# Performance work log

Hardware: AMD Instinct MI355X
Metric: run time of the kernel (lower is better)

Reference implementation:

```python
import jax, jax.numpy as jnp
import numpy as np

TAU = 2.0
SUR_ALPHA = 4.0  # spikingjelly surrogate.Sigmoid default alpha
LN_EPS = 1e-5
SCALE = 0.125
NUM_HEADS = 16


@jax.custom_vjp
def _spike(u):
    return (u >= 0.0).astype(u.dtype)

def _spike_fwd(u):
    return _spike(u), u

def _spike_bwd(u, g):
    s = jax.nn.sigmoid(SUR_ALPHA * u)
    return (g * SUR_ALPHA * s * (1.0 - s),)

_spike.defvjp(_spike_fwd, _spike_bwd)


def lif(x, v_th=1.0):
    # Single-step LIF from fresh state v=0, v_reset=0:
    # v_post = v + (x - v)/tau = x/tau; spike = H(v_post - v_th)
    return _spike(x / TAU - v_th)


def ln(x, g, b):
    m = jnp.mean(x, axis=-1, keepdims=True)
    v = jnp.var(x, axis=-1, keepdims=True)
    return (x - m) * jax.lax.rsqrt(v + LN_EPS) * g + b


def setup_inputs() -> dict:
    key = jax.random.key(0)
    ks = jax.random.split(key, 8)
    B, L, D = 4, 1024, 1024
    HID = 4096
    s_d = 1.0 / np.sqrt(D)
    s_h = 1.0 / np.sqrt(HID)
    return {
        "x": jax.random.normal(ks[0], (B, L, D), jnp.float32),
        "q_w": jax.random.normal(ks[1], (D, D), jnp.float32) * s_d,
        "q_g": jnp.ones((D,), jnp.float32),
        "q_b": jnp.zeros((D,), jnp.float32),
        "k_w": jax.random.normal(ks[2], (D, D), jnp.float32) * s_d,
        "k_g": jnp.ones((D,), jnp.float32),
        "k_b": jnp.zeros((D,), jnp.float32),
        "v_w": jax.random.normal(ks[3], (D, D), jnp.float32) * s_d,
        "v_g": jnp.ones((D,), jnp.float32),
        "v_b": jnp.zeros((D,), jnp.float32),
        "proj_w": jax.random.normal(ks[4], (D, D), jnp.float32) * s_d,
        "proj_bias": jnp.zeros((D,), jnp.float32),
        "proj_g": jnp.ones((D,), jnp.float32),
        "proj_beta": jnp.zeros((D,), jnp.float32),
        "fc1_w": jax.random.normal(ks[5], (D, HID), jnp.float32) * s_d,
        "fc1_bias": jnp.zeros((HID,), jnp.float32),
        "fc1_g": jnp.ones((HID,), jnp.float32),
        "fc1_beta": jnp.zeros((HID,), jnp.float32),
        "fc2_w": jax.random.normal(ks[6], (HID, D), jnp.float32) * s_h,
        "fc2_bias": jnp.zeros((D,), jnp.float32),
        "fc2_g": jnp.ones((D,), jnp.float32),
        "fc2_beta": jnp.zeros((D,), jnp.float32),
    }


def reference(x, q_w, q_g, q_b, k_w, k_g, k_b, v_w, v_g, v_b,
              proj_w, proj_bias, proj_g, proj_beta,
              fc1_w, fc1_bias, fc1_g, fc1_beta,
              fc2_w, fc2_bias, fc2_g, fc2_beta):
    B, L, D = x.shape
    H = NUM_HEADS
    hd = D // H

    # --- SSA ---
    q = lif(ln(x @ q_w, q_g, q_b))  # (B,L,D), binary spikes
    k = lif(ln(x @ k_w, k_g, k_b))
    v = lif(ln(x @ v_w, v_g, v_b))
    q = q.reshape(B, L, H, hd).transpose(0, 2, 1, 3)  # (B,H,L,hd)
    k = k.reshape(B, L, H, hd).transpose(0, 2, 1, 3)
    v = v.reshape(B, L, H, hd).transpose(0, 2, 1, 3)

    attn = jnp.einsum('bhqd,bhkd->bhqk', q, k) * SCALE  # no softmax
    y = jnp.einsum('bhqk,bhkd->bhqd', attn, v)
    y = y.transpose(0, 2, 1, 3).reshape(B, L, D)
    y = lif(y, v_th=0.5)                    # attn_lif (v_threshold=0.5)
    y = lif(ln(y @ proj_w + proj_bias, proj_g, proj_beta))

    x = x + y  # residual 1

    # --- MLP ---
    m = lif(ln(x @ fc1_w + fc1_bias, fc1_g, fc1_beta))
    m = lif(ln(m @ fc2_w + fc2_bias, fc2_g, fc2_beta))

    return x + m  # residual 2
```

## Files before the change

### kernel.cpp

```cpp
#include <hip/hip_runtime.h>
#include <hip/hip_bf16.h>


#define NB 4
#define LL 1024
#define DIM 1024
#define NH 16
#define HDIM 64
#define HID 4096
#define NROWS (NB * LL)

typedef unsigned short u16;
typedef __attribute__((ext_vector_type(8))) short short8v;
typedef __attribute__((ext_vector_type(4))) float f32x4;

__device__ __forceinline__ u16 f2bf(float f) {
    unsigned u = __builtin_bit_cast(unsigned, f);
    return (u16)((u + 0x7fffu + ((u >> 16) & 1u)) >> 16);
}
__device__ __forceinline__ float bf2f(u16 h) {
    unsigned u = ((unsigned)h) << 16;
    return __builtin_bit_cast(float, u);
}
__device__ __forceinline__ void split3v(float v, u16& a, u16& b, u16& c) {
    a = f2bf(v);
    float r = v - bf2f(a);
    b = f2bf(r);
    float r2 = r - bf2f(b);
    c = f2bf(r2);
}

__global__ __launch_bounds__(256) void split3_rows(
    const float* __restrict__ X, u16* __restrict__ Xs, int K)
{
    const int row = blockIdx.y;
    const int c4 = (blockIdx.x * 256 + threadIdx.x) * 4;
    if (c4 >= K) return;
    float4 v = *(const float4*)(X + (size_t)row * K + c4);
    float vv[4] = {v.x, v.y, v.z, v.w};
    u16 h0[4], h1[4], h2[4];
#pragma unroll
    for (int j = 0; j < 4; ++j) split3v(vv[j], h0[j], h1[j], h2[j]);
    u16* base = Xs + (size_t)row * 3 * K + c4;
    *(uint2*)(base + 0 * K) = *(uint2*)h0;
    *(uint2*)(base + 1 * K) = *(uint2*)h1;
    *(uint2*)(base + 2 * K) = *(uint2*)h2;
}

__global__ __launch_bounds__(256) void split_wt(
    const float* __restrict__ W, u16* __restrict__ Wt, int K, int N, int ldwt)
{
    __shared__ float tile[64][65];
    const int k0 = blockIdx.y * 64, n0 = blockIdx.x * 64;
    const int t = threadIdx.x;
    const int rr = t >> 4;
    const int cc = (t & 15) * 4;
#pragma unroll
    for (int it = 0; it < 4; ++it) {
        const int k = rr + it * 16;
        float4 v = *(const float4*)(W + (size_t)(k0 + k) * N + n0 + cc);
        tile[cc + 0][k] = v.x; tile[cc + 1][k] = v.y;
        tile[cc + 2][k] = v.z; tile[cc + 3][k] = v.w;
    }
    __syncthreads();
    const int n = t >> 2, kc = (t & 3) * 16;
    u16 h0[16], h1[16], h2[16];
#pragma unroll
    for (int j = 0; j < 16; ++j)
        split3v(tile[n][kc + j], h0[j], h1[j], h2[j]);
    u16* base = Wt + (size_t)(n0 + n) * ldwt + k0 + kc;
    *(uint4*)(base + 0 * K)     = ((uint4*)h0)[0];
    *(uint4*)(base + 0 * K + 8) = ((uint4*)h0)[1];
    *(uint4*)(base + 1 * K)     = ((uint4*)h1)[0];
    *(uint4*)(base + 1 * K + 8) = ((uint4*)h1)[1];
    *(uint4*)(base + 2 * K)     = ((uint4*)h2)[0];
    *(uint4*)(base + 2 * K + 8) = ((uint4*)h2)[1];
}

#define AS1G const __attribute__((address_space(1))) void*
#define AS3L __attribute__((address_space(3))) void*

__global__ __launch_bounds__(512, 2) void gemm256(
    const u16* __restrict__ A, int lda,
    const u16* __restrict__ Bt, int ldb,
    unsigned apack, unsigned bpack, int nt,
    const float* __restrict__ bias,
    float* __restrict__ Out, int ldo)
{
    __shared__ u16 As2[2][16384];
    __shared__ u16 Bs2[2][16384];
    const int t = threadIdx.x;
    const int wid = t >> 6, lane = t & 63;
    const int wm = wid >> 2, wn = wid & 3;
    int bid = blockIdx.y * gridDim.x + blockIdx.x;
    const int nwg = gridDim.x * gridDim.y;
    bid = (bid & 7) * (nwg >> 3) + (bid >> 3);
    const int row0 = (bid / gridDim.x) * 256, col0 = (bid % gridDim.x) * 256;
    const int lrow = lane & 15, lk = lane >> 4;
    const int sr0 = t >> 3;
    const int scol = ((t & 7) ^ (sr0 & 7)) * 8;

    f32x4 acc[8][4];
#pragma unroll
    for (int i = 0; i < 8; ++i)
#pragma unroll
        for (int j = 0; j < 4; ++j) acc[i][j] = f32x4{0.f, 0.f, 0.f, 0.f};
    short8v afA[4][2], afB[4][2], bf[2][2];

#define STA(bs, Rb, c0)                                                        \
    __builtin_amdgcn_global_load_lds(                                          \
        (AS1G)(A + (size_t)(row0 + (Rb) + sr0) * lda + (c0) + scol),           \
        (AS3L)(&As2[bs][(Rb) * 64 + t * 8]), 16, 0, 0);
#define STB(bs, Rb, c0)                                                        \
    {                                                                          \
        const int _rho = (Rb) + sr0;                                           \
        const int _bc = ((_rho >> 5) & 3) * 64 + ((_rho >> 7) << 5) + (_rho & 31); \
        __builtin_amdgcn_global_load_lds(                                      \
            (AS1G)(Bt + (size_t)(col0 + _bc) * ldb + (c0) + scol),             \
            (AS3L)(&Bs2[bs][(Rb) * 64 + t * 8]), 16, 0, 0);                    \
    }
#define STPAIR0(bs, cA, cB) STA(bs, 0, cA)   STA(bs, 128, cA)
#define STPAIR1(bs, cA, cB) STB(bs, 0, cB)   STB(bs, 64, cB)
#define STPAIR2(bs, cA, cB) STA(bs, 64, cA)  STA(bs, 192, cA)
#define STPAIR3(bs, cA, cB) STB(bs, 128, cB) STB(bs, 192, cB)

#define VMW(n) asm volatile("s_waitcnt vmcnt(" #n ")" ::: "memory");
#define BAR  __builtin_amdgcn_s_barrier();
#define BARP                                                                   \
    __builtin_amdgcn_s_barrier();                                              \
    __builtin_amdgcn_sched_barrier(0);
#define LGKM0                                                                  \
    asm volatile("s_waitcnt lgkmcnt(0)" ::: "memory");                         \
    __builtin_amdgcn_sched_barrier(0);

#define LDA(dst, MQ, P)                                                        \
    _Pragma("unroll")                                                          \
    for (int mf = 0; mf < 4; ++mf) {                                           \
        const int r = wm * 128 + (MQ) * 64 + mf * 16 + lrow;                   \
        _Pragma("unroll")                                                      \
        for (int ks = 0; ks < 2; ++ks) {                                       \
            const int slot = (lk + ks * 4) ^ (r & 7);                          \
            dst[mf][ks] = *(const short8v*)&As2[P][r * 64 + slot * 8];         \
        }                                                                      \
    }
#define LDB(NQ, P)                                                             \
    _Pragma("unroll")                                                          \
    for (int nf = 0; nf < 2; ++nf) {                                           \
        const int rho = (NQ) * 128 + (wn >> 1) * 64 + (wn & 1) * 32            \
                        + nf * 16 + lrow;                                      \
        _Pragma("unroll")                                                      \
        for (int ks = 0; ks < 2; ++ks) {                                       \
            const int slot = (lk + ks * 4) ^ (rho & 7);                        \
            bf[nf][ks] = *(const short8v*)&Bs2[P][rho * 64 + slot * 8];        \
        }                                                                      \
    }
#define MM(asrc, MQ, NQ)                                                       \
    __builtin_amdgcn_s_setprio(1);                                             \
    _Pragma("unroll")                                                          \
    for (int mf = 0; mf < 4; ++mf)                                             \
        _Pragma("unroll")                                                      \
        for (int nf = 0; nf < 2; ++nf)                                         \
            _Pragma("unroll")                                                  \
            for (int ks = 0; ks < 2; ++ks)                                     \
                acc[(MQ) * 4 + mf][(NQ) * 2 + nf] =                            \
                    __builtin_amdgcn_mfma_f32_16x16x32_bf16(                   \
                        asrc[mf][ks], bf[nf][ks],                              \
                        acc[(MQ) * 4 + mf][(NQ) * 2 + nf], 0, 0, 0);           \
    __builtin_amdgcn_s_setprio(0);

    {
        const int cA = (apack & 15) * 1024;
        const int cB = (bpack & 15) * 1024;
        STPAIR0(0, cA, cB) STPAIR1(0, cA, cB)
        STPAIR2(0, cA, cB) STPAIR3(0, cA, cB)
    }

    for (int kt = 0; kt < nt - 1; ++kt) {
        const int p = kt & 1, np = p ^ 1;
        const int nkt = kt + 1;
        const int nns = nkt >> 4, nk0 = (nkt & 15) * 64;
        const int nA = (int)((apack >> (nns * 4)) & 15) * 1024 + nk0;
        const int nB = (int)((bpack >> (nns * 4)) & 15) * 1024 + nk0;
        VMW(4) BARP
        LDA(afA, 0, p) LDB(0, p) STPAIR0(np, nA, nB) LGKM0 MM(afA, 0, 0)
        VMW(4) BAR
        LDA(afB, 1, p) STPAIR1(np, nA, nB) LGKM0 MM(afB, 1, 0)
        VMW(4) BAR
        LDB(1, p) STPAIR2(np, nA, nB) LGKM0 MM(afB, 1, 1)
        BAR
        STPAIR3(np, nA, nB) MM(afA, 0, 1)
    }
    {
        const int p = (nt - 1) & 1;
        VMW(4) BARP LDA(afA, 0, p) LDB(0, p) LGKM0 MM(afA, 0, 0)
        VMW(2) BAR  LDA(afB, 1, p) LGKM0 MM(afB, 1, 0)
        VMW(0) BAR  LDB(1, p) LGKM0 MM(afB, 1, 1)
        BAR         MM(afA, 0, 1)
    }
#undef STA
#undef STB
#undef STPAIR0
#undef STPAIR1
#undef STPAIR2
#undef STPAIR3
#undef VMW
#undef BAR
#undef BARP
#undef LGKM0
#undef LDA
#undef LDB
#undef MM

#pragma unroll
    for (int ni = 0; ni < 4; ++ni) {
        const int col = col0 + wn * 64 + ni * 16 + lrow;
        const float bv = bias ? bias[col] : 0.f;
#pragma unroll
        for (int mi = 0; mi < 8; ++mi) {
            const int rbase = row0 + wm * 128 + mi * 16 + lk * 4;
#pragma unroll
            for (int r = 0; r < 4; ++r)
                Out[(size_t)(rbase + r) * ldo + col] = acc[mi][ni][r] + bv;
        }
    }
}

struct SegList { int a[6]; int b[6]; int n; };

template <int BN_>
__global__ __launch_bounds__(256) void gemm_mfma(
    const u16* __restrict__ A, int lda,
    const u16* __restrict__ Bt, int ldb,
    SegList segs, int Kseg,
    const float* __restrict__ bias,
    float* __restrict__ Out, int ldo)
{
    constexpr int NF = BN_ / 32;
    __shared__ u16 As[128 * 64];
    __shared__ u16 Bs[BN_ * 64];
    const int t = threadIdx.x;
    const int wid = t >> 6, lane = t & 63;
    const int wr = wid >> 1, wc = wid & 1;
    int bid = blockIdx.y * gridDim.x + blockIdx.x;
    const int nwg = gridDim.x * gridDim.y;
    bid = (bid & 7) * (nwg >> 3) + (bid >> 3);
    const int row0 = (bid / gridDim.x) * 128, col0 = (bid % gridDim.x) * BN_;
    const int lrow = lane & 15;
    const int s_subrow = lane >> 3;
    const int s_slot   = (lane & 7) ^ (lane >> 3);
    const int s_coff   = s_slot * 8;

    f32x4 acc[4][NF];
#pragma unroll
    for (int i = 0; i < 4; ++i)
#pragma unroll
        for (int j = 0; j < NF; ++j) acc[i][j] = f32x4{0.f, 0.f, 0.f, 0.f};

    for (int s = 0; s < segs.n; ++s) {
        const u16* pa = A + segs.a[s];
        const u16* pb = Bt + segs.b[s];
        for (int k0 = 0; k0 < Kseg; k0 += 64) {
            asm volatile("s_waitcnt lgkmcnt(0)" ::: "memory");
            __syncthreads();
#pragma unroll
            for (int c = 0; c < 4; ++c) {
                const int chunk = wid * 4 + c;
                const int rg = row0 + chunk * 8 + s_subrow;
                __builtin_amdgcn_global_load_lds(
                    (AS1G)(pa + (size_t)rg * lda + k0 + s_coff),
                    (AS3L)(&As[chunk * 512 + lane * 8]), 16, 0, 0);
            }
#pragma unroll
            for (int c = 0; c < NF; ++c) {
                const int chunk = wid * NF + c;
                const int rg = col0 + chunk * 8 + s_subrow;
                __builtin_amdgcn_global_load_lds(
                    (AS1G)(pb + (size_t)rg * ldb + k0 + s_coff),
                    (AS3L)(&Bs[chunk * 512 + lane * 8]), 16, 0, 0);
            }
            asm volatile("s_waitcnt vmcnt(0)" ::: "memory");
            __syncthreads();
#pragma unroll
            for (int ksub = 0; ksub < 2; ++ksub) {
                short8v af[4], bfr[NF];
#pragma unroll
                for (int f = 0; f < 4; ++f) {
                    const int ra = wr * 64 + f * 16 + lrow;
                    const int slot = ((lane >> 4) + ksub * 4) ^ (lrow & 7);
                    af[f] = *(const short8v*)&As[ra * 64 + slot * 8];
                }
#pragma unroll
                for (int f = 0; f < NF; ++f) {
                    const int rb = wc * (BN_ / 2) + f * 16 + lrow;
                    const int slot = ((lane >> 4) + ksub * 4) ^ (lrow & 7);
                    bfr[f] = *(const short8v*)&Bs[rb * 64 + slot * 8];
                }
#pragma unroll
                for (int i = 0; i < 4; ++i)
#pragma unroll
                    for (int j = 0; j < NF; ++j)
                        acc[i][j] = __builtin_amdgcn_mfma_f32_16x16x32_bf16(
                            af[i], bfr[j], acc[i][j], 0, 0, 0);
            }
        }
    }
#pragma unroll
    for (int j = 0; j < NF; ++j) {
        const int col = col0 + wc * (BN_ / 2) + j * 16 + lrow;
        const float bv = bias ? bias[col] : 0.f;
#pragma unroll
        for (int i = 0; i < 4; ++i) {
            const int rbase = row0 + wr * 64 + i * 16 + (lane >> 4) * 4;
#pragma unroll
            for (int r = 0; r < 4; ++r)
                Out[(size_t)(rbase + r) * ldo + col] = acc[i][j][r] + bv;
        }
    }
}

template <int DN>
__global__ __launch_bounds__(256) void lnlif2(
    const float* __restrict__ U, int ld, int coloff,
    const float* __restrict__ g, const float* __restrict__ beta,
    const float* __restrict__ resid,
    u16* __restrict__ spike_bf16,
    float* __restrict__ out_f32,
    u16* __restrict__ split3_out)
{
    constexpr int PT = DN / 1024;
    const int r = blockIdx.x, t = threadIdx.x;
    const float4* u4 = (const float4*)(U + (size_t)r * ld + coloff);
    float4 vals[PT];
    float lsum = 0.f;
#pragma unroll
    for (int i = 0; i < PT; ++i) {
        vals[i] = u4[t + i * 256];
        lsum += (vals[i].x + vals[i].y) + (vals[i].z + vals[i].w);
    }
    __shared__ float red[4];
    __shared__ float bcast;
    for (int o = 32; o > 0; o >>= 1) lsum += __shfl_down(lsum, o);
    if ((t & 63) == 0) red[t >> 6] = lsum;
    __syncthreads();
    if (t == 0) bcast = (red[0] + red[1] + red[2] + red[3]) * (1.f / DN);
    __syncthreads();
    const float m = bcast;
    float lss = 0.f;
#pragma unroll
    for (int i = 0; i < PT; ++i) {
        float dx = vals[i].x - m, dy = vals[i].y - m;
        float dz = vals[i].z - m, dw = vals[i].w - m;
        lss += (dx * dx + dy * dy) + (dz * dz + dw * dw);
    }
    for (int o = 32; o > 0; o >>= 1) lss += __shfl_down(lss, o);
    if ((t & 63) == 0) red[t >> 6] = lss;
    __syncthreads();
    if (t == 0) bcast = (red[0] + red[1] + red[2] + red[3]) * (1.f / DN);
    __syncthreads();
    const float rs = 1.f / sqrtf(bcast + 1e-5f);
#pragma unroll
    for (int i = 0; i < PT; ++i) {
        const int c = (t + i * 256) * 4;
        const size_t idx = (size_t)r * DN + c;
        const float4 gg = *(const float4*)(g + c);
        const float4 bb = *(const float4*)(beta + c);
        float sv[4];
        sv[0] = ((vals[i].x - m) * rs * gg.x + bb.x >= 2.0f) ? 1.f : 0.f;
        sv[1] = ((vals[i].y - m) * rs * gg.y + bb.y >= 2.0f) ? 1.f : 0.f;
        sv[2] = ((vals[i].z - m) * rs * gg.z + bb.z >= 2.0f) ? 1.f : 0.f;
        sv[3] = ((vals[i].w - m) * rs * gg.w + bb.w >= 2.0f) ? 1.f : 0.f;
        if (spike_bf16) {
            u16 sp[4];
#pragma unroll
            for (int j = 0; j < 4; ++j) sp[j] = sv[j] != 0.f ? (u16)0x3F80 : (u16)0;
            *(uint2*)(spike_bf16 + idx) = *(uint2*)sp;
        }
        if (out_f32 || split3_out) {
            float4 rv = resid ? *(const float4*)(resid + idx)
                              : float4{0.f, 0.f, 0.f, 0.f};
            float vv[4] = {rv.x + sv[0], rv.y + sv[1], rv.z + sv[2], rv.w + sv[3]};
            if (out_f32) {
                float4 ov = {vv[0], vv[1], vv[2], vv[3]};
                *(float4*)(out_f32 + idx) = ov;
            }
            if (split3_out) {
                u16 h0[4], h1[4], h2[4];
#pragma unroll
                for (int j = 0; j < 4; ++j) split3v(vv[j], h0[j], h1[j], h2[j]);
                u16* base = split3_out + (size_t)r * 3 * DN + c;
                *(uint2*)(base + 0 * DN) = *(uint2*)h0;
                *(uint2*)(base + 1 * DN) = *(uint2*)h1;
                *(uint2*)(base + 2 * DN) = *(uint2*)h2;
            }
        }
    }
}

__global__ __launch_bounds__(256) void ktv_part(
    const u16* __restrict__ Sk, const u16* __restrict__ Sv,
    float* __restrict__ ktvp)
{
    const int bh = blockIdx.x, ck = blockIdx.y;
    const int b = bh >> 4, h = bh & 15;
    __shared__ float kch[64][64];
    __shared__ float vch[64][64];
    const int t = threadIdx.x;
    const int i = t >> 2;
    const int j0 = (t & 3) << 4;
    float4 a0 = {0,0,0,0}, a1 = {0,0,0,0}, a2 = {0,0,0,0}, a3 = {0,0,0,0};
    for (int l0 = ck * 256; l0 < ck * 256 + 256; l0 += 64) {
        __syncthreads();
#pragma unroll
        for (int q = 0; q < 2; ++q) {
            const int chunk = t + q * 256;
            const int li = chunk >> 3, c8 = (chunk & 7) << 3;
            const size_t off = ((size_t)b * LL + l0 + li) * DIM + h * HDIM + c8;
            union { uint4 v; u16 s[8]; } uk, uv;
            uk.v = *(const uint4*)(Sk + off);
            uv.v = *(const uint4*)(Sv + off);
#pragma unroll
            for (int j = 0; j < 8; ++j) {
                kch[li][c8 + j] = uk.s[j] ? 1.f : 0.f;
                vch[li][c8 + j] = uv.s[j] ? 1.f : 0.f;
            }
        }
        __syncthreads();
        for (int l = 0; l < 64; ++l) {
            if (kch[l][i] != 0.f) {
                const float4 v0 = *(float4*)&vch[l][j0];
                const float4 v1 = *(float4*)&vch[l][j0 + 4];
                const float4 v2 = *(float4*)&vch[l][j0 + 8];
                const float4 v3 = *(float4*)&vch[l][j0 + 12];
                a0.x += v0.x; a0.y += v0.y; a0.z += v0.z; a0.w += v0.w;
                a1.x += v1.x; a1.y += v1.y; a1.z += v1.z; a1.w += v1.w;
                a2.x += v2.x; a2.y += v2.y; a2.z += v2.z; a2.w += v2.w;
                a3.x += v3.x; a3.y += v3.y; a3.z += v3.z; a3.w += v3.w;
            }
        }
    }
    const size_t o = (((size_t)ck * 64 + bh) * 64 + i) * 64 + j0;
    *(float4*)(ktvp + o)      = a0;
    *(float4*)(ktvp + o + 4)  = a1;
    *(float4*)(ktvp + o + 8)  = a2;
    *(float4*)(ktvp + o + 12) = a3;
}

__global__ __launch_bounds__(256) void qktv_bf16(
    const u16* __restrict__ Sq, const float* __restrict__ ktvp,
    u16* __restrict__ Y)
{
    const int bh = blockIdx.x, ck = blockIdx.y;
    const int b = bh >> 4, h = bh & 15;
    __shared__ float kt[64][64];
    const int t = threadIdx.x;
#pragma unroll
    for (int q = 0; q < 16; ++q) {
        const int idx = t + q * 256;
        ((float*)kt)[idx] = (ktvp[((size_t)0 * 64 + bh) * 4096 + idx]
                           + ktvp[((size_t)1 * 64 + bh) * 4096 + idx])
                          + (ktvp[((size_t)2 * 64 + bh) * 4096 + idx]
                           + ktvp[((size_t)3 * 64 + bh) * 4096 + idx]);
    }
    __syncthreads();
    const int li = t >> 6;
    const int j = t & 63;
    for (int l0 = ck * 128; l0 < ck * 128 + 128; l0 += 4) {
        const size_t roff = ((size_t)b * LL + l0 + li) * DIM + h * HDIM;
        const u16 sqv = Sq[roff + j];
        unsigned long long mask = __ballot(sqv != 0);
        float acc = 0.f;
        while (mask) {
            const int i = __ffsll((unsigned long long)mask) - 1;
            mask &= mask - 1;
            acc += kt[i][j];
        }
        const float y = 0.125f * acc;
        Y[roff + j] = (y >= 1.0f) ? (u16)0x3F80 : (u16)0;
    }
}

#define BM 128
#define BN 128
#define BK 16

__global__ __launch_bounds__(256) void gemm_f32(
    const float* __restrict__ A, const float* __restrict__ W,
    const float* __restrict__ bias, float* __restrict__ U,
    int M, int K, int N)
{
    __shared__ float As[BK][BM];
    __shared__ float Bs[BK][BN];
    const int t = threadIdx.x;
    const int tx = t & 15, ty = t >> 4;
    const int row0 = blockIdx.y * BM, col0 = blockIdx.x * BN;
    const int ar = t >> 2;
    const int ac = (t & 3) << 2;
    const int br = t >> 5;
    const int bc = (t & 31) << 2;
    float acc[8][8];
#pragma unroll
    for (int i = 0; i < 8; ++i)
#pragma unroll
        for (int j = 0; j < 8; ++j) acc[i][j] = 0.f;
    for (int k0 = 0; k0 < K; k0 += BK) {
        float4 va0 = *(const float4*)(A + (size_t)(row0 + ar) * K + k0 + ac);
        float4 va1 = *(const float4*)(A + (size_t)(row0 + ar + 64) * K + k0 + ac);
        float4 vb0 = *(const float4*)(W + (size_t)(k0 + br) * N + col0 + bc);
        float4 vb1 = *(const float4*)(W + (size_t)(k0 + br + 8) * N + col0 + bc);
        __syncthreads();
        As[ac + 0][ar] = va0.x; As[ac + 1][ar] = va0.y;
        As[ac + 2][ar] = va0.z; As[ac + 3][ar] = va0.w;
        As[ac + 0][ar + 64] = va1.x; As[ac + 1][ar + 64] = va1.y;
        As[ac + 2][ar + 64] = va1.z; As[ac + 3][ar + 64] = va1.w;
        *(float4*)&Bs[br][bc] = vb0;
        *(float4*)&Bs[br + 8][bc] = vb1;
        __syncthreads();
#pragma unroll
        for (int kk = 0; kk < BK; ++kk) {
            float4 fa0 = *(float4*)&As[kk][ty * 8];
            float4 fa1 = *(float4*)&As[kk][ty * 8 + 4];
            float4 fb0 = *(float4*)&Bs[kk][tx * 8];
            float4 fb1 = *(float4*)&Bs[kk][tx * 8 + 4];
            float av[8] = {fa0.x, fa0.y, fa0.z, fa0.w, fa1.x, fa1.y, fa1.z, fa1.w};
            float bv[8] = {fb0.x, fb0.y, fb0.z, fb0.w, fb1.x, fb1.y, fb1.z, fb1.w};
#pragma unroll
            for (int i = 0; i < 8; ++i)
#pragma unroll
                for (int j = 0; j < 8; ++j)
                    acc[i][j] += av[i] * bv[j];
        }
    }
    float bvals[8];
#pragma unroll
    for (int j = 0; j < 8; ++j)
        bvals[j] = bias ? bias[col0 + tx * 8 + j] : 0.f;
#pragma unroll
    for (int i = 0; i < 8; ++i) {
        const int row = row0 + ty * 8 + i;
        float* dst = U + (size_t)row * N + col0 + tx * 8;
        float4 o0, o1;
        o0.x = acc[i][0] + bvals[0]; o0.y = acc[i][1] + bvals[1];
        o0.z = acc[i][2] + bvals[2]; o0.w = acc[i][3] + bvals[3];
        o1.x = acc[i][4] + bvals[4]; o1.y = acc[i][5] + bvals[5];
        o1.z = acc[i][6] + bvals[6]; o1.w = acc[i][7] + bvals[7];
        *(float4*)dst = o0;
        *(float4*)(dst + 4) = o1;
    }
}

template <int DN>
__global__ __launch_bounds__(256) void lnlif_old(
    const float* __restrict__ U, const float* __restrict__ g,
    const float* __restrict__ beta, float thr,
    const float* __restrict__ resid, float* __restrict__ out)
{
    constexpr int PT = DN / 256;
    const int r = blockIdx.x, t = threadIdx.x;
    const float* u = U + (size_t)r * DN;
    float vals[PT];
    float lsum = 0.f;
#pragma unroll
    for (int i = 0; i < PT; ++i) { vals[i] = u[t + i * 256]; lsum += vals[i]; }
    __shared__ float red[4];
    __shared__ float bc0;
    for (int o = 32; o > 0; o >>= 1) lsum += __shfl_down(lsum, o);
    if ((t & 63) == 0) red[t >> 6] = lsum;
    __syncthreads();
    if (t == 0) bc0 = (red[0] + red[1] + red[2] + red[3]) * (1.f / DN);
    __syncthreads();
    const float m = bc0;
    float lss = 0.f;
#pragma unroll
    for (int i = 0; i < PT; ++i) { float d = vals[i] - m; lss += d * d; }
    for (int o = 32; o > 0; o >>= 1) lss += __shfl_down(lss, o);
    if ((t & 63) == 0) red[t >> 6] = lss;
    __syncthreads();
    if (t == 0) bc0 = (red[0] + red[1] + red[2] + red[3]) * (1.f / DN);
    __syncthreads();
    const float rs = 1.0f / sqrtf(bc0 + 1e-5f);
#pragma unroll
    for (int i = 0; i < PT; ++i) {
        const int c = t + i * 256;
        const float nrm = (vals[i] - m) * rs * g[c] + beta[c];
        const float s = (nrm >= thr) ? 1.0f : 0.0f;
        out[(size_t)r * DN + c] = resid ? (resid[(size_t)r * DN + c] + s) : s;
    }
}

__global__ __launch_bounds__(256) void ktv_f32(
    const float* __restrict__ Sk, const float* __restrict__ Sv,
    float* __restrict__ ktvb)
{
    const int bh = blockIdx.x;
    const int b = bh >> 4, h = bh & 15;
    __shared__ float kch[64][64];
    __shared__ float vch[64][64];
    const int t = threadIdx.x;
    const int i = t >> 2;
    const int j0 = (t & 3) << 4;
    float4 a0 = {0,0,0,0}, a1 = {0,0,0,0}, a2 = {0,0,0,0}, a3 = {0,0,0,0};
    for (int l0 = 0; l0 < LL; l0 += 64) {
        __syncthreads();
#pragma unroll
        for (int q = 0; q < 4; ++q) {
            const int idx = t + q * 256;
            const int li = idx >> 4, c4 = (idx & 15) << 2;
            const size_t off = ((size_t)b * LL + l0 + li) * DIM + h * HDIM + c4;
            *(float4*)&kch[li][c4] = *(const float4*)(Sk + off);
            *(float4*)&vch[li][c4] = *(const float4*)(Sv + off);
        }
        __syncthreads();
        for (int l = 0; l < 64; ++l) {
            if (kch[l][i] != 0.f) {
                const float4 v0 = *(float4*)&vch[l][j0];
                const float4 v1 = *(float4*)&vch[l][j0 + 4];
                const float4 v2 = *(float4*)&vch[l][j0 + 8];
                const float4 v3 = *(float4*)&vch[l][j0 + 12];
                a0.x += v0.x; a0.y += v0.y; a0.z += v0.z; a0.w += v0.w;
                a1.x += v1.x; a1.y += v1.y; a1.z += v1.z; a1.w += v1.w;
                a2.x += v2.x; a2.y += v2.y; a2.z += v2.z; a2.w += v2.w;
                a3.x += v3.x; a3.y += v3.y; a3.z += v3.z; a3.w += v3.w;
            }
        }
    }
    const size_t o = ((size_t)bh * 64 + i) * 64 + j0;
    *(float4*)(ktvb + o)      = a0;
    *(float4*)(ktvb + o + 4)  = a1;
    *(float4*)(ktvb + o + 8)  = a2;
    *(float4*)(ktvb + o + 12) = a3;
}

__global__ __launch_bounds__(256) void qktv_f32(
    const float* __restrict__ Sq, const float* __restrict__ ktvb,
    float* __restrict__ Y)
{
    const int bh = blockIdx.x;
    const int b = bh >> 4, h = bh & 15;
    __shared__ float kt[64][64];
    const int t = threadIdx.x;
#pragma unroll
    for (int q = 0; q < 16; ++q) {
        const int idx = t + q * 256;
        ((float*)kt)[idx] = ktvb[(size_t)bh * 4096 + idx];
    }
    __syncthreads();
    const int li = t >> 6;
    const int j = t & 63;
    for (int l0 = 0; l0 < LL; l0 += 4) {
        const size_t roff = ((size_t)b * LL + l0 + li) * DIM + h * HDIM;
        const float sqv = Sq[roff + j];
        unsigned long long mask = __ballot(sqv != 0.f);
        float acc = 0.f;
        while (mask) {
            const int i = __ffsll((unsigned long long)mask) - 1;
            mask &= mask - 1;
            acc += kt[i][j];
        }
        const float y = 0.125f * acc;
        Y[roff + j] = (y >= 1.0f) ? 1.0f : 0.0f;
    }
}

extern "C" void kernel_launch(void* const* d_in, const int* in_sizes, int n_in,
                              void* d_out, int out_size, void* d_ws, size_t ws_size,
                              hipStream_t stream)
{
    const float* x        = (const float*)d_in[0];
    const float* q_w      = (const float*)d_in[1];
    const float* q_g      = (const float*)d_in[2];
    const float* q_b      = (const float*)d_in[3];
    const float* k_w      = (const float*)d_in[4];
    const float* k_g      = (const float*)d_in[5];
    const float* k_b      = (const float*)d_in[6];
    const float* v_w      = (const float*)d_in[7];
    const float* v_g      = (const float*)d_in[8];
    const float* v_b      = (const float*)d_in[9];
    const float* proj_w   = (const float*)d_in[10];
    const float* proj_bias= (const float*)d_in[11];
    const float* proj_g   = (const float*)d_in[12];
    const float* proj_beta= (const float*)d_in[13];
    const float* fc1_w    = (const float*)d_in[14];
    const float* fc1_bias = (const float*)d_in[15];
    const float* fc1_g    = (const float*)d_in[16];
    const float* fc1_beta = (const float*)d_in[17];
    const float* fc2_w    = (const float*)d_in[18];
    const float* fc2_bias = (const float*)d_in[19];
    const float* fc2_g    = (const float*)d_in[20];
    const float* fc2_beta = (const float*)d_in[21];

    const dim3 blk(256);
    const size_t NEEDED = 143654912;

    if (ws_size >= NEEDED) {
        char* ws = (char*)d_ws;
        float* U    = (float*)ws;
        u16*   Xsh  = (u16*)(ws + 67108864);
        u16*   Wbuf = (u16*)(ws + 100663296);
        u16*   Sq   = (u16*)(ws + 125829120);
        u16*   Sk   = (u16*)(ws + 134217728);
        u16*   SvYb = (u16*)((char*)Xsh + 25165824);
        u16*   Xs   = Xsh;
        u16*   X1s  = Xsh;
        u16*   Sm   = Xsh;
        float* X1   = (float*)d_out;
        float* ktvp = (float*)(ws + 100663296);

        const int pa6[6] = {0, 1, 2, 0, 1, 0}, pb6[6] = {0, 1, 0, 2, 0, 1};
        unsigned apack = 0, bpack = 0;
        for (int i = 0; i < 6; ++i) {
            apack |= (unsigned)pa6[i] << (4 * i);
            bpack |= (unsigned)pb6[i] << (4 * i);
        }
        SegList segP;
        {
            for (int i = 0; i < 6; ++i) { segP.a[i] = 0; segP.b[i] = 0; }
            segP.b[1] = 1024; segP.b[2] = 2048; segP.n = 3;
        }
        SegList segF2;
        {
            for (int i = 0; i < 6; ++i) { segF2.a[i] = 0; segF2.b[i] = 0; }
            segF2.b[1] = 4096; segF2.b[2] = 8192; segF2.n = 3;
        }

        split3_rows<<<dim3(1, NROWS), blk, 0, stream>>>(x, Xs, DIM);

        split_wt<<<dim3(16, 16), blk, 0, stream>>>(q_w, Wbuf,               DIM, DIM, 3072);
        split_wt<<<dim3(16, 16), blk, 0, stream>>>(k_w, Wbuf + 1024 * 3072, DIM, DIM, 3072);
        split_wt<<<dim3(16, 16), blk, 0, stream>>>(v_w, Wbuf + 2048 * 3072, DIM, DIM, 3072);
        gemm256<<<dim3(12, 16), dim3(512), 0, stream>>>(
            Xs, 3072, Wbuf, 3072, apack, bpack, 96, nullptr, U, 3072);
        lnlif2<DIM><<<NROWS, blk, 0, stream>>>(U, 3072, 0,    q_g, q_b, nullptr, Sq,   nullptr, nullptr);
        lnlif2<DIM><<<NROWS, blk, 0, stream>>>(U, 3072, 1024, k_g, k_b, nullptr, Sk,   nullptr, nullptr);
        lnlif2<DIM><<<NROWS, blk, 0, stream>>>(U, 3072, 2048, v_g, v_b, nullptr, SvYb, nullptr, nullptr);

        ktv_part<<<dim3(NB * NH, 4), blk, 0, stream>>>(Sk, SvYb, ktvp);
        qktv_bf16<<<dim3(NB * NH, 8), blk, 0, stream>>>(Sq, ktvp, SvYb);

        split_wt<<<dim3(16, 16), blk, 0, stream>>>(proj_w, Wbuf, DIM, DIM, 3072);
        gemm_mfma<128><<<dim3(8, 32), blk, 0, stream>>>(SvYb, 1024, Wbuf, 3072, segP, 1024, proj_bias, U, DIM);
        lnlif2<DIM><<<NROWS, blk, 0, stream>>>(U, DIM, 0, proj_g, proj_beta, x, nullptr, X1, X1s);

        split_wt<<<dim3(64, 16), blk, 0, stream>>>(fc1_w, Wbuf, DIM, HID, 3072);
        gemm256<<<dim3(16, 16), dim3(512), 0, stream>>>(
            X1s, 3072, Wbuf, 3072, apack, bpack, 96, fc1_bias, U, HID);
        lnlif2<HID><<<NROWS, blk, 0, stream>>>(U, HID, 0, fc1_g, fc1_beta, nullptr, Sm, nullptr, nullptr);

        split_wt<<<dim3(16, 64), blk, 0, stream>>>(fc2_w, Wbuf, HID, DIM, 12288);
        gemm_mfma<128><<<dim3(8, 32), blk, 0, stream>>>(Sm, 4096, Wbuf, 12288, segF2, 4096, fc2_bias, U, DIM);
        lnlif2<DIM><<<NROWS, blk, 0, stream>>>(U, DIM, 0, fc2_g, fc2_beta, X1, nullptr, (float*)d_out, nullptr);
        return;
    }

    float* U    = (float*)d_ws;
    float* Sq   = U + (size_t)1 * NROWS * DIM;
    float* Sk   = U + (size_t)2 * NROWS * DIM;
    float* Sv   = U + (size_t)3 * NROWS * DIM;
    float* Yb   = Sv;
    float* ktvb = U + (size_t)NROWS * HID;
    float* Y2   = ktvb + (size_t)NB * NH * HDIM * HDIM;
    float* X1   = (float*)d_out;
    float* outf = (float*)d_out;

    const dim3 gemm_d(DIM / BN, NROWS / BM);
    const dim3 gemm_h(HID / BN, NROWS / BM);

    gemm_f32<<<gemm_d, blk, 0, stream>>>(x, q_w, nullptr, U, NROWS, DIM, DIM);
    lnlif_old<DIM><<<NROWS, blk, 0, stream>>>(U, q_g, q_b, 2.0f, nullptr, Sq);
    gemm_f32<<<gemm_d, blk, 0, stream>>>(x, k_w, nullptr, U, NROWS, DIM, DIM);
    lnlif_old<DIM><<<NROWS, blk, 0, stream>>>(U, k_g, k_b, 2.0f, nullptr, Sk);
    gemm_f32<<<gemm_d, blk, 0, stream>>>(x, v_w, nullptr, U, NROWS, DIM, DIM);
    lnlif_old<DIM><<<NROWS, blk, 0, stream>>>(U, v_g, v_b, 2.0f, nullptr, Sv);

    ktv_f32<<<NB * NH, blk, 0, stream>>>(Sk, Sv, ktvb);
    qktv_f32<<<NB * NH, blk, 0, stream>>>(Sq, ktvb, Yb);

    gemm_f32<<<gemm_d, blk, 0, stream>>>(Yb, proj_w, proj_bias, U, NROWS, DIM, DIM);
    lnlif_old<DIM><<<NROWS, blk, 0, stream>>>(U, proj_g, proj_beta, 2.0f, x, X1);

    gemm_f32<<<gemm_h, blk, 0, stream>>>(X1, fc1_w, fc1_bias, U, NROWS, DIM, HID);
    lnlif_old<HID><<<NROWS, blk, 0, stream>>>(U, fc1_g, fc1_beta, 2.0f, nullptr, U);

    gemm_f32<<<gemm_d, blk, 0, stream>>>(U, fc2_w, fc2_bias, Y2, NROWS, HID, DIM);
    lnlif_old<DIM><<<NROWS, blk, 0, stream>>>(Y2, fc2_g, fc2_beta, 2.0f, X1, outf);
}
```

Baseline: 686.6 us.

## Replace proj/fc2 GEMM with double-buffered 128x128 pipelined MFMA kernel

Swaps the simple single-buffered gemm_mfma used for the proj and fc2 spike GEMMs for a new gemm128p kernel. The new kernel double-buffers LDS and interleaves async global-to-LDS loads for the next K tile with MFMA work on the current one, using split vmcnt waits, s_setprio and sched barriers, as the gemm256 kernel already does. Segment offsets are packed into a bitfield so the three bf16 weight splits are walked as one continuous K loop. It doubles LDS use per block and adds scheduling complexity, which may lower occupancy.

```diff
diff --git a/kernel.cpp b/kernel.cpp
--- a/kernel.cpp
+++ b/kernel.cpp
@@ -197,16 +197,156 @@
         VMW(0) BAR  LDB(1, p) LGKM0 MM(afB, 1, 1)
         BAR         MM(afA, 0, 1)
     }
-#undef STA
-#undef STB
 #undef STPAIR0
 #undef STPAIR1
 #undef STPAIR2
 #undef STPAIR3
+#undef LDA
+#undef LDB
+#undef MM
+
+#pragma unroll
+    for (int ni = 0; ni < 4; ++ni) {
+        const int col = col0 + wn * 64 + ni * 16 + lrow;
+        const float bv = bias ? bias[col] : 0.f;
+#pragma unroll
+        for (int mi = 0; mi < 8; ++mi) {
+            const int rbase = row0 + wm * 128 + mi * 16 + lk * 4;
+#pragma unroll
+            for (int r = 0; r < 4; ++r)
+                Out[(size_t)(rbase + r) * ldo + col] = acc[mi][ni][r] + bv;
+        }
+    }
+#undef STA
+#undef STB
 #undef VMW
 #undef BAR
 #undef BARP
 #undef LGKM0
+}
+
+__global__ __launch_bounds__(256) void gemm128p(
+    const u16* __restrict__ A, int lda,
+    const u16* __restrict__ Bt, int ldb,
+    unsigned apack, unsigned bpack, int nt, int tpsLog,
+    const float* __restrict__ bias,
+    float* __restrict__ Out, int ldo)
+{
+    __shared__ u16 As2[2][8192];
+    __shared__ u16 Bs2[2][8192];
+    const int t = threadIdx.x;
+    const int wid = t >> 6, lane = t & 63;
+    const int wm = wid >> 1, wn = wid & 1;
+    int bid = blockIdx.y * gridDim.x + blockIdx.x;
+    const int nwg = gridDim.x * gridDim.y;
+    bid = (bid & 7) * (nwg >> 3) + (bid >> 3);
+    const int row0 = (bid / gridDim.x) * 128, col0 = (bid % gridDim.x) * 128;
+    const int lrow = lane & 15, lk = lane >> 4;
+    const int sr0 = t >> 3;
+    const int scol = ((t & 7) ^ (sr0 & 7)) * 8;
+    const int segK = 64 << tpsLog;
+    const int tmask = (1 << tpsLog) - 1;
+
+    f32x4 acc[4][4];
+#pragma unroll
+    for (int i = 0; i < 4; ++i)
+#pragma unroll
+        for (int j = 0; j < 4; ++j) acc[i][j] = f32x4{0.f, 0.f, 0.f, 0.f};
+    short8v afA[2][2], afB[2][2], bf[2][2];
+
+#define STA(bs, Rb, c0)                                                        \
+    __builtin_amdgcn_global_load_lds(                                          \
+        (AS1G)(A + (size_t)(row0 + (Rb) + sr0) * lda + (c0) + scol),           \
+        (AS3L)(&As2[bs][(Rb) * 64 + t * 8]), 16, 0, 0);
+#define STB(bs, Rb, c0)                                                        \
+    {                                                                          \
+        const int _rho = (Rb) + sr0;                                           \
+        const int _bc = ((_rho >> 5) & 1) * 64 + ((_rho >> 6) << 5) + (_rho & 31); \
+        __builtin_amdgcn_global_load_lds(                                      \
+            (AS1G)(Bt + (size_t)(col0 + _bc) * ldb + (c0) + scol),             \
+            (AS3L)(&Bs2[bs][(Rb) * 64 + t * 8]), 16, 0, 0);                    \
+    }
+#define STPAIR0(bs, cA, cB) STA(bs, 0, cA)  STA(bs, 64, cA)
+#define STPAIR1(bs, cA, cB) STB(bs, 0, cB)  STB(bs, 32, cB)
+#define STPAIR2(bs, cA, cB) STA(bs, 32, cA) STA(bs, 96, cA)
+#define STPAIR3(bs, cA, cB) STB(bs, 64, cB) STB(bs, 96, cB)
+
+#define VMW(n) asm volatile("s_waitcnt vmcnt(" #n ")" ::: "memory");
+#define BAR  __builtin_amdgcn_s_barrier();
+#define BARP                                                                   \
+    __builtin_amdgcn_s_barrier();                                              \
+    __builtin_amdgcn_sched_barrier(0);
+#define LGKM0                                                                  \
+    asm volatile("s_waitcnt lgkmcnt(0)" ::: "memory");                         \
+    __builtin_amdgcn_sched_barrier(0);
+
+#define LDA(dst, MQ, P)                                                        \
+    _Pragma("unroll")                                                          \
+    for (int mf = 0; mf < 2; ++mf) {                                           \
+        const int r = wm * 64 + (MQ) * 32 + mf * 16 + lrow;                    \
+        _Pragma("unroll")                                                      \
+        for (int ks = 0; ks < 2; ++ks) {                                       \
+            const int slot = (lk + ks * 4) ^ (r & 7);                          \
+            dst[mf][ks] = *(const short8v*)&As2[P][r * 64 + slot * 8];         \
+        }                                                                      \
+    }
+#define LDB(NQ, P)                                                             \
+    _Pragma("unroll")                                                          \
+    for (int nf = 0; nf < 2; ++nf) {                                           \
+        const int rho = (NQ) * 64 + wn * 32 + nf * 16 + lrow;                  \
+        _Pragma("unroll")                                                      \
+        for (int ks = 0; ks < 2; ++ks) {                                       \
+            const int slot = (lk + ks * 4) ^ (rho & 7);                        \
+            bf[nf][ks] = *(const short8v*)&Bs2[P][rho * 64 + slot * 8];        \
+        }                                                                      \
+    }
+#define MM(asrc, MQ, NQ)                                                       \
+    __builtin_amdgcn_s_setprio(1);                                             \
+    _Pragma("unroll")                                                          \
+    for (int mf = 0; mf < 2; ++mf)                                             \
+        _Pragma("unroll")                                                      \
+        for (int nf = 0; nf < 2; ++nf)                                         \
+            _Pragma("unroll")                                                  \
+            for (int ks = 0; ks < 2; ++ks)                                     \
+                acc[(MQ) * 2 + mf][(NQ) * 2 + nf] =                            \
+                    __builtin_amdgcn_mfma_f32_16x16x32_bf16(                   \
+                        asrc[mf][ks], bf[nf][ks],                              \
+                        acc[(MQ) * 2 + mf][(NQ) * 2 + nf], 0, 0, 0);           \
+    __builtin_amdgcn_s_setprio(0);
+
+    {
+        const int cA = (apack & 15) * segK;
+        const int cB = (bpack & 15) * segK;
+        STPAIR0(0, cA, cB) STPAIR1(0, cA, cB)
+        STPAIR2(0, cA, cB) STPAIR3(0, cA, cB)
+    }
+
+    for (int kt = 0; kt < nt - 1; ++kt) {
+        const int p = kt & 1, np = p ^ 1;
+        const int nkt = kt + 1;
+        const int nns = nkt >> tpsLog, nk0 = (nkt & tmask) * 64;
+        const int nA = (int)((apack >> (nns * 4)) & 15) * segK + nk0;
+        const int nB = (int)((bpack >> (nns * 4)) & 15) * segK + nk0;
+        VMW(4) BARP
+        LDA(afA, 0, p) LDB(0, p) STPAIR0(np, nA, nB) LGKM0 MM(afA, 0, 0)
+        VMW(4) BAR
+        LDA(afB, 1, p) STPAIR1(np, nA, nB) LGKM0 MM(afB, 1, 0)
+        VMW(4) BAR
+        LDB(1, p) STPAIR2(np, nA, nB) LGKM0 MM(afB, 1, 1)
+        BAR
+        STPAIR3(np, nA, nB) MM(afA, 0, 1)
+    }
+    {
+        const int p = (nt - 1) & 1;
+        VMW(4) BARP LDA(afA, 0, p) LDB(0, p) LGKM0 MM(afA, 0, 0)
+        VMW(2) BAR  LDA(afB, 1, p) LGKM0 MM(afB, 1, 0)
+        VMW(0) BAR  LDB(1, p) LGKM0 MM(afB, 1, 1)
+        BAR         MM(afA, 0, 1)
+    }
+#undef STPAIR0
+#undef STPAIR1
+#undef STPAIR2
+#undef STPAIR3
 #undef LDA
 #undef LDB
 #undef MM
@@ -216,106 +356,19 @@
         const int col = col0 + wn * 64 + ni * 16 + lrow;
         const float bv = bias ? bias[col] : 0.f;
 #pragma unroll
-        for (int mi = 0; mi < 8; ++mi) {
-            const int rbase = row0 + wm * 128 + mi * 16 + lk * 4;
+        for (int mi = 0; mi < 4; ++mi) {
+            const int rbase = row0 + wm * 64 + mi * 16 + lk * 4;
 #pragma unroll
             for (int r = 0; r < 4; ++r)
                 Out[(size_t)(rbase + r) * ldo + col] = acc[mi][ni][r] + bv;
         }
     }
-}
-
-struct SegList { int a[6]; int b[6]; int n; };
-
-template <int BN_>
-__global__ __launch_bounds__(256) void gemm_mfma(
-    const u16* __restrict__ A, int lda,
-    const u16* __restrict__ Bt, int ldb,
-    SegList segs, int Kseg,
-    const float* __restrict__ bias,
-    float* __restrict__ Out, int ldo)
-{
-    constexpr int NF = BN_ / 32;
-    __shared__ u16 As[128 * 64];
-    __shared__ u16 Bs[BN_ * 64];
-    const int t = threadIdx.x;
-    const int wid = t >> 6, lane = t & 63;
-    const int wr = wid >> 1, wc = wid & 1;
-    int bid = blockIdx.y * gridDim.x + blockIdx.x;
-    const int nwg = gridDim.x * gridDim.y;
-    bid = (bid & 7) * (nwg >> 3) + (bid >> 3);
-    const int row0 = (bid / gridDim.x) * 128, col0 = (bid % gridDim.x) * BN_;
-    const int lrow = lane & 15;
-    const int s_subrow = lane >> 3;
-    const int s_slot   = (lane & 7) ^ (lane >> 3);
-    const int s_coff   = s_slot * 8;
-
-    f32x4 acc[4][NF];
-#pragma unroll
-    for (int i = 0; i < 4; ++i)
-#pragma unroll
-        for (int j = 0; j < NF; ++j) acc[i][j] = f32x4{0.f, 0.f, 0.f, 0.f};
-
-    for (int s = 0; s < segs.n; ++s) {
-        const u16* pa = A + segs.a[s];
-        const u16* pb = Bt + segs.b[s];
-        for (int k0 = 0; k0 < Kseg; k0 += 64) {
-            asm volatile("s_waitcnt lgkmcnt(0)" ::: "memory");
-            __syncthreads();
-#pragma unroll
-            for (int c = 0; c < 4; ++c) {
-                const int chunk = wid * 4 + c;
-                const int rg = row0 + chunk * 8 + s_subrow;
-                __builtin_amdgcn_global_load_lds(
-                    (AS1G)(pa + (size_t)rg * lda + k0 + s_coff),
-                    (AS3L)(&As[chunk * 512 + lane * 8]), 16, 0, 0);
-            }
-#pragma unroll
-            for (int c = 0; c < NF; ++c) {
-                const int chunk = wid * NF + c;
-                const int rg = col0 + chunk * 8 + s_subrow;
-                __builtin_amdgcn_global_load_lds(
-                    (AS1G)(pb + (size_t)rg * ldb + k0 + s_coff),
-                    (AS3L)(&Bs[chunk * 512 + lane * 8]), 16, 0, 0);
-            }
-            asm volatile("s_waitcnt vmcnt(0)" ::: "memory");
-            __syncthreads();
-#pragma unroll
-            for (int ksub = 0; ksub < 2; ++ksub) {
-                short8v af[4], bfr[NF];
-#pragma unroll
-                for (int f = 0; f < 4; ++f) {
-                    const int ra = wr * 64 + f * 16 + lrow;
-                    const int slot = ((lane >> 4) + ksub * 4) ^ (lrow & 7);
-                    af[f] = *(const short8v*)&As[ra * 64 + slot * 8];
-                }
-#pragma unroll
-                for (int f = 0; f < NF; ++f) {
-                    const int rb = wc * (BN_ / 2) + f * 16 + lrow;
-                    const int slot = ((lane >> 4) + ksub * 4) ^ (lrow & 7);
-                    bfr[f] = *(const short8v*)&Bs[rb * 64 + slot * 8];
-                }
-#pragma unroll
-                for (int i = 0; i < 4; ++i)
-#pragma unroll
-                    for (int j = 0; j < NF; ++j)
-                        acc[i][j] = __builtin_amdgcn_mfma_f32_16x16x32_bf16(
-                            af[i], bfr[j], acc[i][j], 0, 0, 0);
-            }
-        }
-    }
-#pragma unroll
-    for (int j = 0; j < NF; ++j) {
-        const int col = col0 + wc * (BN_ / 2) + j * 16 + lrow;
-        const float bv = bias ? bias[col] : 0.f;
-#pragma unroll
-        for (int i = 0; i < 4; ++i) {
-            const int rbase = row0 + wr * 64 + i * 16 + (lane >> 4) * 4;
-#pragma unroll
-            for (int r = 0; r < 4; ++r)
-                Out[(size_t)(rbase + r) * ldo + col] = acc[i][j][r] + bv;
-        }
-    }
+#undef STA
+#undef STB
+#undef VMW
+#undef BAR
+#undef BARP
+#undef LGKM0
 }
 
 template <int DN>
@@ -711,16 +764,7 @@
             apack |= (unsigned)pa6[i] << (4 * i);
             bpack |= (unsigned)pb6[i] << (4 * i);
         }
-        SegList segP;
-        {
-            for (int i = 0; i < 6; ++i) { segP.a[i] = 0; segP.b[i] = 0; }
-            segP.b[1] = 1024; segP.b[2] = 2048; segP.n = 3;
-        }
-        SegList segF2;
-        {
-            for (int i = 0; i < 6; ++i) { segF2.a[i] = 0; segF2.b[i] = 0; }
-            segF2.b[1] = 4096; segF2.b[2] = 8192; segF2.n = 3;
-        }
+        const unsigned spk_a = 0u, spk_b = 0x210u;
 
         split3_rows<<<dim3(1, NROWS), blk, 0, stream>>>(x, Xs, DIM);
 
@@ -737,7 +781,8 @@
         qktv_bf16<<<dim3(NB * NH, 8), blk, 0, stream>>>(Sq, ktvp, SvYb);
 
         split_wt<<<dim3(16, 16), blk, 0, stream>>>(proj_w, Wbuf, DIM, DIM, 3072);
-        gemm_mfma<128><<<dim3(8, 32), blk, 0, stream>>>(SvYb, 1024, Wbuf, 3072, segP, 1024, proj_bias, U, DIM);
+        gemm128p<<<dim3(8, 32), blk, 0, stream>>>(
+            SvYb, 1024, Wbuf, 3072, spk_a, spk_b, 48, 4, proj_bias, U, DIM);
         lnlif2<DIM><<<NROWS, blk, 0, stream>>>(U, DIM, 0, proj_g, proj_beta, x, nullptr, X1, X1s);
 
         split_wt<<<dim3(64, 16), blk, 0, stream>>>(fc1_w, Wbuf, DIM, HID, 3072);
@@ -746,7 +791,8 @@
         lnlif2<HID><<<NROWS, blk, 0, stream>>>(U, HID, 0, fc1_g, fc1_beta, nullptr, Sm, nullptr, nullptr);
 
         split_wt<<<dim3(16, 64), blk, 0, stream>>>(fc2_w, Wbuf, HID, DIM, 12288);
-        gemm_mfma<128><<<dim3(8, 32), blk, 0, stream>>>(Sm, 4096, Wbuf, 12288, segF2, 4096, fc2_bias, U, DIM);
+        gemm128p<<<dim3(8, 32), blk, 0, stream>>>(
+            Sm, 4096, Wbuf, 12288, spk_a, spk_b, 192, 6, fc2_bias, U, DIM);
         lnlif2<DIM><<<NROWS, blk, 0, stream>>>(U, DIM, 0, fc2_g, fc2_beta, X1, nullptr, (float*)d_out, nullptr);
         return;
     }
```

After: 720.5 us. 4.9% more time.

## Split-K the proj and fc2 GEMMs and sum partials in the LN+LIF kernel

Applied to the files above, without the earlier changes.

The proj and fc2 GEMMs now use a narrower 64-column tile and a two-way split-K over blockIdx.z. Each half writes its own fp32 partial output, and only the first half adds the bias. The following LN+LIF kernel gains a second input pointer and adds the two partials while loading. This raises the workgroup count from 256 to 1024 so the GPU is better filled, at the cost of an extra fp32 partial buffer write and read. It also moves the epilogue store loop in gemm256 ahead of some macro undefs, which has no speed effect.

```diff
diff --git a/kernel.cpp b/kernel.cpp
--- a/kernel.cpp
+++ b/kernel.cpp
@@ -197,32 +197,32 @@
         VMW(0) BAR  LDB(1, p) LGKM0 MM(afB, 1, 1)
         BAR         MM(afA, 0, 1)
     }
-#undef STA
-#undef STB
 #undef STPAIR0
 #undef STPAIR1
 #undef STPAIR2
 #undef STPAIR3
+#undef LDA
+#undef LDB
+#undef MM
+
+#pragma unroll
+    for (int ni = 0; ni < 4; ++ni) {
+        const int col = col0 + wn * 64 + ni * 16 + lrow;
+        const float bv = bias ? bias[col] : 0.f;
+#pragma unroll
+        for (int mi = 0; mi < 8; ++mi) {
+            const int rbase = row0 + wm * 128 + mi * 16 + lk * 4;
+#pragma unroll
+            for (int r = 0; r < 4; ++r)
+                Out[(size_t)(rbase + r) * ldo + col] = acc[mi][ni][r] + bv;
+        }
+    }
+#undef STA
+#undef STB
 #undef VMW
 #undef BAR
 #undef BARP
 #undef LGKM0
-#undef LDA
-#undef LDB
-#undef MM
-
-#pragma unroll
-    for (int ni = 0; ni < 4; ++ni) {
-        const int col = col0 + wn * 64 + ni * 16 + lrow;
-        const float bv = bias ? bias[col] : 0.f;
-#pragma unroll
-        for (int mi = 0; mi < 8; ++mi) {
-            const int rbase = row0 + wm * 128 + mi * 16 + lk * 4;
-#pragma unroll
-            for (int r = 0; r < 4; ++r)
-                Out[(size_t)(rbase + r) * ldo + col] = acc[mi][ni][r] + bv;
-        }
-    }
 }
 
 struct SegList { int a[6]; int b[6]; int n; };
@@ -241,6 +241,9 @@
     const int t = threadIdx.x;
     const int wid = t >> 6, lane = t & 63;
     const int wr = wid >> 1, wc = wid & 1;
+    const int z = blockIdx.z;
+    const int koff = z * Kseg;
+    Out += (size_t)z * (size_t)gridDim.y * 128 * ldo;
     int bid = blockIdx.y * gridDim.x + blockIdx.x;
     const int nwg = gridDim.x * gridDim.y;
     bid = (bid & 7) * (nwg >> 3) + (bid >> 3);
@@ -257,8 +260,8 @@
         for (int j = 0; j < NF; ++j) acc[i][j] = f32x4{0.f, 0.f, 0.f, 0.f};
 
     for (int s = 0; s < segs.n; ++s) {
-        const u16* pa = A + segs.a[s];
-        const u16* pb = Bt + segs.b[s];
+        const u16* pa = A + segs.a[s] + koff;
+        const u16* pb = Bt + segs.b[s] + koff;
         for (int k0 = 0; k0 < Kseg; k0 += 64) {
             asm volatile("s_waitcnt lgkmcnt(0)" ::: "memory");
             __syncthreads();
@@ -307,7 +310,7 @@
 #pragma unroll
     for (int j = 0; j < NF; ++j) {
         const int col = col0 + wc * (BN_ / 2) + j * 16 + lrow;
-        const float bv = bias ? bias[col] : 0.f;
+        const float bv = (bias && z == 0) ? bias[col] : 0.f;
 #pragma unroll
         for (int i = 0; i < 4; ++i) {
             const int rbase = row0 + wr * 64 + i * 16 + (lane >> 4) * 4;
@@ -320,7 +323,7 @@
 
 template <int DN>
 __global__ __launch_bounds__(256) void lnlif2(
-    const float* __restrict__ U, int ld, int coloff,
+    const float* __restrict__ U, const float* __restrict__ U2, int ld, int coloff,
     const float* __restrict__ g, const float* __restrict__ beta,
     const float* __restrict__ resid,
     u16* __restrict__ spike_bf16,
@@ -330,11 +333,17 @@
     constexpr int PT = DN / 1024;
     const int r = blockIdx.x, t = threadIdx.x;
     const float4* u4 = (const float4*)(U + (size_t)r * ld + coloff);
+    const float4* u24 = U2 ? (const float4*)(U2 + (size_t)r * ld + coloff) : nullptr;
     float4 vals[PT];
     float lsum = 0.f;
 #pragma unroll
     for (int i = 0; i < PT; ++i) {
         vals[i] = u4[t + i * 256];
+        if (u24) {
+            float4 w = u24[t + i * 256];
+            vals[i].x += w.x; vals[i].y += w.y;
+            vals[i].z += w.z; vals[i].w += w.w;
+        }
         lsum += (vals[i].x + vals[i].y) + (vals[i].z + vals[i].w);
     }
     __shared__ float red[4];
@@ -694,6 +703,7 @@
     if (ws_size >= NEEDED) {
         char* ws = (char*)d_ws;
         float* U    = (float*)ws;
+        float* Up2  = U + (size_t)NROWS * DIM;
         u16*   Xsh  = (u16*)(ws + 67108864);
         u16*   Wbuf = (u16*)(ws + 100663296);
         u16*   Sq   = (u16*)(ws + 125829120);
@@ -729,25 +739,27 @@
         split_wt<<<dim3(16, 16), blk, 0, stream>>>(v_w, Wbuf + 2048 * 3072, DIM, DIM, 3072);
         gemm256<<<dim3(12, 16), dim3(512), 0, stream>>>(
             Xs, 3072, Wbuf, 3072, apack, bpack, 96, nullptr, U, 3072);
-        lnlif2<DIM><<<NROWS, blk, 0, stream>>>(U, 3072, 0,    q_g, q_b, nullptr, Sq,   nullptr, nullptr);
-        lnlif2<DIM><<<NROWS, blk, 0, stream>>>(U, 3072, 1024, k_g, k_b, nullptr, Sk,   nullptr, nullptr);
-        lnlif2<DIM><<<NROWS, blk, 0, stream>>>(U, 3072, 2048, v_g, v_b, nullptr, SvYb, nullptr, nullptr);
+        lnlif2<DIM><<<NROWS, blk, 0, stream>>>(U, nullptr, 3072, 0,    q_g, q_b, nullptr, Sq,   nullptr, nullptr);
+        lnlif2<DIM><<<NROWS, blk, 0, stream>>>(U, nullptr, 3072, 1024, k_g, k_b, nullptr, Sk,   nullptr, nullptr);
+        lnlif2<DIM><<<NROWS, blk, 0, stream>>>(U, nullptr, 3072, 2048, v_g, v_b, nullptr, SvYb, nullptr, nullptr);
 
         ktv_part<<<dim3(NB * NH, 4), blk, 0, stream>>>(Sk, SvYb, ktvp);
         qktv_bf16<<<dim3(NB * NH, 8), blk, 0, stream>>>(Sq, ktvp, SvYb);
 
         split_wt<<<dim3(16, 16), blk, 0, stream>>>(proj_w, Wbuf, DIM, DIM, 3072);
-        gemm_mfma<128><<<dim3(8, 32), blk, 0, stream>>>(SvYb, 1024, Wbuf, 3072, segP, 1024, proj_bias, U, DIM);
-        lnlif2<DIM><<<NROWS, blk, 0, stream>>>(U, DIM, 0, proj_g, proj_beta, x, nullptr, X1, X1s);
+        gemm_mfma<64><<<dim3(16, 32, 2), blk, 0, stream>>>(
+            SvYb, 1024, Wbuf, 3072, segP, 512, proj_bias, U, DIM);
+        lnlif2<DIM><<<NROWS, blk, 0, stream>>>(U, Up2, DIM, 0, proj_g, proj_beta, x, nullptr, X1, X1s);
 
         split_wt<<<dim3(64, 16), blk, 0, stream>>>(fc1_w, Wbuf, DIM, HID, 3072);
         gemm256<<<dim3(16, 16), dim3(512), 0, stream>>>(
             X1s, 3072, Wbuf, 3072, apack, bpack, 96, fc1_bias, U, HID);
-        lnlif2<HID><<<NROWS, blk, 0, stream>>>(U, HID, 0, fc1_g, fc1_beta, nullptr, Sm, nullptr, nullptr);
+        lnlif2<HID><<<NROWS, blk, 0, stream>>>(U, nullptr, HID, 0, fc1_g, fc1_beta, nullptr, Sm, nullptr, nullptr);
 
         split_wt<<<dim3(16, 64), blk, 0, stream>>>(fc2_w, Wbuf, HID, DIM, 12288);
-        gemm_mfma<128><<<dim3(8, 32), blk, 0, stream>>>(Sm, 4096, Wbuf, 12288, segF2, 4096, fc2_bias, U, DIM);
-        lnlif2<DIM><<<NROWS, blk, 0, stream>>>(U, DIM, 0, fc2_g, fc2_beta, X1, nullptr, (float*)d_out, nullptr);
+        gemm_mfma<64><<<dim3(16, 32, 2), blk, 0, stream>>>(
+            Sm, 4096, Wbuf, 12288, segF2, 2048, fc2_bias, U, DIM);
+        lnlif2<DIM><<<NROWS, blk, 0, stream>>>(U, Up2, DIM, 0, fc2_g, fc2_beta, X1, nullptr, (float*)d_out, nullptr);
         return;
     }
 
```

Measured after the change: 589.1 us. 14.2% less time.
